# Optimization experiments

Hardware: AMD Instinct MI355X
Metric: run time of the kernel (lower is better)

The kernel has to match this reference:

```python
import jax, jax.numpy as jnp
import numpy as np
from jax import lax

B, L, DIM = 2, 2048, 2048
HK, HV = 16, 32
DK, DV = 128, 128
KCONV = 4
KEY_DIM = HK * DK          # 2048
VAL_DIM = HV * DV          # 4096
CONV_DIM = 2 * KEY_DIM + VAL_DIM  # 8192
EPS = 1e-6


def _l2norm(x, eps=1e-6):
    return x * lax.rsqrt((x * x).sum(-1, keepdims=True) + eps)


def _gated_delta_rule(q, k, v, g, beta):
    # q,k: (B,L,H,DK); v: (B,L,H,DV); g,beta: (B,L,H)
    q = _l2norm(q.astype(jnp.float32)) * (DK ** -0.5)
    k = _l2norm(k.astype(jnp.float32))
    v = v.astype(jnp.float32)
    g = g.astype(jnp.float32)
    beta = beta.astype(jnp.float32)
    # time-major for scan: (L,B,H,...)
    qs = q.transpose(1, 0, 2, 3)
    ks = k.transpose(1, 0, 2, 3)
    vs = v.transpose(1, 0, 2, 3)
    gs = g.transpose(1, 0, 2)
    bs = beta.transpose(1, 0, 2)
    state0 = jnp.zeros((B, HV, DK, DV), jnp.float32)

    def step(state, inp):
        q_t, k_t, v_t, g_t, b_t = inp
        state = state * jnp.exp(g_t)[..., None, None]          # decay
        kv_mem = jnp.einsum('bhk,bhkv->bhv', k_t, state)       # read
        delta = (v_t - kv_mem) * b_t[..., None]                # error-correct
        state = state + jnp.einsum('bhk,bhv->bhkv', k_t, delta)
        out_t = jnp.einsum('bhk,bhkv->bhv', q_t, state)
        return state, out_t

    _, outs = lax.scan(step, state0, (qs, ks, vs, gs, bs))
    return outs.transpose(1, 0, 2, 3)  # (B,L,H,DV)


def setup_inputs() -> dict:
    key = jax.random.key(0)
    ks = jax.random.split(key, 8)
    s = 0.02
    return {
        'x': jax.random.normal(ks[0], (B, L, DIM), jnp.float32),
        'W_qkv': jax.random.normal(ks[1], (CONV_DIM, DIM), jnp.float32) * s,
        'W_z': jax.random.normal(ks[2], (VAL_DIM, DIM), jnp.float32) * s,
        'W_a': jax.random.normal(ks[3], (HV, DIM), jnp.float32) * s,
        'W_b': jax.random.normal(ks[4], (HV, DIM), jnp.float32) * s,
        'conv_w': jax.random.normal(ks[5], (CONV_DIM, 1, KCONV), jnp.float32) * 0.2,
        'A_log': jnp.log(jax.random.uniform(ks[6], (HV,), jnp.float32, 1e-6, 16.0)),
        'dt_bias': jnp.ones((HV,), jnp.float32),
        'norm_weight': jnp.ones((DV,), jnp.float32),
        'W_out': jax.random.normal(ks[7], (DIM, VAL_DIM), jnp.float32) * s,
    }


def reference(x, W_qkv, W_z, W_a, W_b, conv_w, A_log, dt_bias, norm_weight, W_out):
    qkv = x @ W_qkv.T                      # (B,L,CONV_DIM)
    z = x @ W_z.T                          # (B,L,VAL_DIM)
    a = x @ W_a.T                          # (B,L,HV)
    b = x @ W_b.T                          # (B,L,HV)
    # depthwise causal conv1d (left pad K-1)
    h = qkv.transpose(0, 2, 1)             # (B,C,L)
    h = lax.conv_general_dilated(h, conv_w, window_strides=(1,),
                                 padding=[(KCONV - 1, 0)],
                                 dimension_numbers=('NCH', 'OIH', 'NCH'),
                                 feature_group_count=CONV_DIM)
    qkv = jax.nn.silu(h.transpose(0, 2, 1))
    q, k, v = jnp.split(qkv, [KEY_DIM, 2 * KEY_DIM], axis=-1)
    q = q.reshape(B, L, HK, DK)
    k = k.reshape(B, L, HK, DK)
    v = v.reshape(B, L, HV, DV)
    rep = HV // HK
    if rep > 1:
        q = jnp.repeat(q, rep, axis=2)
        k = jnp.repeat(k, rep, axis=2)
    g = -jnp.exp(A_log.astype(jnp.float32)) * jax.nn.softplus(a.astype(jnp.float32) + dt_bias)
    beta = jax.nn.sigmoid(b)
    out = _gated_delta_rule(q, k, v, g, beta)   # (B,L,HV,DV) fp32
    # gated RMSNorm over DV: silu(z) * weight * norm(out)
    var = (out * out).mean(-1, keepdims=True)
    out = out * lax.rsqrt(var + EPS) * norm_weight
    zg = z.reshape(B, L, HV, DV)
    out = out * jax.nn.silu(zg.astype(jnp.float32))
    out = out.astype(x.dtype).reshape(B, L, VAL_DIM)
    return out @ W_out.T
```

## Files before the change

### kernel.cpp

```cpp
#include <hip/hip_runtime.h>
#include <hip/hip_bf16.h>
#include <cstddef>
#include <cstdint>

constexpr int B = 2, L = 2048, DIM = 2048;
constexpr int HK = 16, HV = 32, DK = 128, DV = 128;
constexpr int KEY_DIM = HK * DK;
constexpr int VAL_DIM = HV * DV;
constexpr int CONV_DIM = 2 * KEY_DIM + VAL_DIM;
constexpr int NPROJ = CONV_DIM + VAL_DIM + HV + HV;
constexpr int NPAD  = ((NPROJ + 255) / 256) * 256;
constexpr size_t ROWS = (size_t)B * L;
constexpr float EPS = 1e-6f;
constexpr int CHUNK = 64, NCHUNK = L / CHUNK;
constexpr int NCH_TOT = B * HV * NCHUNK;
constexpr int CONV_LT = 8;
constexpr int CONV_TL = L / CONV_LT;

constexpr size_t OFF_QKV  = 0;
constexpr size_t OFF_Z    = OFF_QKV + ROWS * CONV_DIM * 2;
constexpr size_t OFF_A    = OFF_Z   + ROWS * VAL_DIM * 2;
constexpr size_t OFF_B    = OFF_A   + ROWS * HV * 4;
constexpr size_t OFF_G    = OFF_B   + ROWS * HV * 4;
constexpr size_t OFF_BETA = OFF_G   + ROWS * HV * 4;
constexpr size_t OFF_U    = OFF_BETA + ROWS * HV * 4;
constexpr size_t OFF_WQK  = OFF_U + (size_t)NCH_TOT * CHUNK * DV * 4;
constexpr size_t OFF_HALO = OFF_WQK + (size_t)NCH_TOT * CHUNK * CHUNK * 2;
constexpr size_t WS_NEED_BYTES = OFF_HALO + (size_t)3 * B * CONV_LT * CONV_DIM * 2;
constexpr size_t OFF_WCAT = OFF_U;
constexpr size_t OFF_XB   = OFF_WQK;
constexpr size_t OFF_WOB  = OFF_U;
static_assert((size_t)NPAD * DIM * 2 <= (size_t)NCH_TOT * CHUNK * DV * 4, "Wcat fits U");

__device__ __forceinline__ float bf2f(unsigned short u) {
    union { float f; uint32_t i; } c; c.i = ((uint32_t)u) << 16; return c.f;
}
__device__ __forceinline__ unsigned short f2bf(float f) {
    union { float f; uint32_t u; } c; c.f = f;
    uint32_t u = c.u + 0x7FFFu + ((c.u >> 16) & 1u);
    return (unsigned short)(u >> 16);
}
__device__ __forceinline__ uint32_t pk2(float a, float b) {
    return (uint32_t)f2bf(a) | ((uint32_t)f2bf(b) << 16);
}

typedef __attribute__((ext_vector_type(8))) short bfrag;
typedef __attribute__((ext_vector_type(4))) float ffrag;

__device__ __forceinline__ void gload16(const unsigned short* g, unsigned short* l) {
    __builtin_amdgcn_global_load_lds(
        (const __attribute__((address_space(1))) uint32_t*)g,
        (__attribute__((address_space(3))) uint32_t*)l, 16, 0, 0);
}

__device__ __forceinline__ const float* w_row_multi(int n, const float* Wq, const float* Wz,
                                                    const float* Wa, const float* Wb) {
    if (n < CONV_DIM)                return Wq + (size_t)n * DIM;
    if (n < CONV_DIM + VAL_DIM)      return Wz + (size_t)(n - CONV_DIM) * DIM;
    if (n < CONV_DIM + VAL_DIM + HV) return Wa + (size_t)(n - CONV_DIM - VAL_DIM) * DIM;
    return Wb + (size_t)(n - CONV_DIM - VAL_DIM - HV) * DIM;
}

__global__ __launch_bounds__(256) void cvt_wcat(
    const float* __restrict__ Wq, const float* __restrict__ Wz,
    const float* __restrict__ Wa, const float* __restrict__ Wb,
    unsigned short* __restrict__ dst)
{
    const int r = blockIdx.x;
    const int c = threadIdx.x * 8;
    uint4 o;
    if (r < NPROJ) {
        const float* s = w_row_multi(r, Wq, Wz, Wa, Wb) + c;
        float4 v0 = *(const float4*)s;
        float4 v1 = *(const float4*)(s + 4);
        o = make_uint4(pk2(v0.x, v0.y), pk2(v0.z, v0.w), pk2(v1.x, v1.y), pk2(v1.z, v1.w));
    } else {
        o = make_uint4(0u, 0u, 0u, 0u);
    }
    *(uint4*)&dst[(size_t)r * DIM + c] = o;
}

__global__ __launch_bounds__(256) void cvt_f32bf(const float* __restrict__ src,
                                                 unsigned short* __restrict__ dst, int cols)
{
    const size_t r = blockIdx.x;
    for (int c = threadIdx.x * 8; c < cols; c += 256 * 8) {
        const float* s = src + r * cols + c;
        float4 v0 = *(const float4*)s;
        float4 v1 = *(const float4*)(s + 4);
        *(uint4*)&dst[r * cols + c] =
            make_uint4(pk2(v0.x, v0.y), pk2(v0.z, v0.w), pk2(v1.x, v1.y), pk2(v1.z, v1.w));
    }
}

__device__ __forceinline__ void store_multi(int m, int n, float v,
                                            unsigned short* qkv, unsigned short* z,
                                            float* a, float* b) {
    if (n < CONV_DIM) {
        qkv[(size_t)m * CONV_DIM + n] = f2bf(v);
    } else if (n < CONV_DIM + VAL_DIM) {
        z[(size_t)m * VAL_DIM + (n - CONV_DIM)] = f2bf(v);
    } else if (n < CONV_DIM + VAL_DIM + HV) {
        a[(size_t)m * HV + (n - CONV_DIM - VAL_DIM)] = v;
    } else if (n < NPROJ) {
        b[(size_t)m * HV + (n - CONV_DIM - VAL_DIM - HV)] = v;
    }
}

constexpr int BK = 64;

__global__ __launch_bounds__(512, 2) void gemm_inproj_bf(
    const unsigned short* __restrict__ xb,
    const unsigned short* __restrict__ Wcat,
    unsigned short* __restrict__ qkv, unsigned short* __restrict__ z,
    float* __restrict__ a_out, float* __restrict__ b_out)
{
    extern __shared__ __align__(16) unsigned short lds[];

    constexpr int NBX = NPAD / 256;
    constexpr int NB  = NBX * 16;
    const int id  = blockIdx.x;
    const int swz = (id & 7) * (NB >> 3) + (id >> 3);
    const int bx  = swz >> 4;
    const int by  = swz & 15;
    const int row0 = by * 256;
    const int col0 = bx * 256;

    const int t = threadIdx.x, lane = t & 63, wid = t >> 6;
    const int wr = wid >> 2, wc = wid & 3;
    const int quad = lane >> 4, l16 = lane & 15;

    ffrag acc[8][4];
#pragma unroll
    for (int i = 0; i < 8; ++i)
#pragma unroll
        for (int j = 0; j < 4; ++j) acc[i][j] = (ffrag)0.f;

    const int srow  = t >> 3;
    const int sslot = t & 7;
    const int scol  = ((sslot ^ (srow & 7)) * 8);
    const unsigned short* aS = xb   + (size_t)(row0 + srow) * DIM + scol;
    const unsigned short* bS = Wcat + (size_t)(col0 + srow) * DIM + scol;
    unsigned short* aD0 = lds + (wid * 8) * 64;
    unsigned short* bD0 = lds + 32768 + (wid * 8) * 64;

    const int x7 = l16 & 7;

    auto STAGE = [&](int buf, int k0) {
        unsigned short* aD = aD0 + buf * 16384;
        unsigned short* bD = bD0 + buf * 16384;
#pragma unroll
        for (int j = 0; j < 4; ++j) {
            gload16(aS + (size_t)(j * 64) * DIM + k0, aD + j * 64 * 64);
            gload16(bS + (size_t)(j * 64) * DIM + k0, bD + j * 64 * 64);
        }
    };

    auto COMPUTE = [&](int buf) {
        const unsigned short* A  = lds + buf * 16384;
        const unsigned short* Bm = lds + 32768 + buf * 16384;
#pragma unroll
        for (int kk = 0; kk < 2; ++kk) {
            const int so = ((kk * 4 + quad) ^ x7) * 8;
            bfrag aF[8], bF[4];
#pragma unroll
            for (int m = 0; m < 8; ++m)
                aF[m] = *(const bfrag*)&A[(wr * 128 + m * 16 + l16) * 64 + so];
#pragma unroll
            for (int n = 0; n < 4; ++n)
                bF[n] = *(const bfrag*)&Bm[(wc * 64 + n * 16 + l16) * 64 + so];
#pragma unroll
            for (int m = 0; m < 8; ++m)
#pragma unroll
                for (int n = 0; n < 4; ++n)
                    acc[m][n] = __builtin_amdgcn_mfma_f32_16x16x32_bf16(
                        aF[m], bF[n], acc[m][n], 0, 0, 0);
        }
    };

    STAGE(0, 0);
    __syncthreads();
    for (int kt = 0; kt < DIM / BK; ++kt) {
        if (kt + 1 < DIM / BK) STAGE((kt + 1) & 1, (kt + 1) * BK);
        COMPUTE(kt & 1);
        __syncthreads();
    }

#pragma unroll
    for (int m = 0; m < 8; ++m)
#pragma unroll
        for (int n = 0; n < 4; ++n) {
            int gr = row0 + wr * 128 + m * 16 + quad * 4;
            int gc = col0 + wc * 64 + n * 16 + l16;
#pragma unroll
            for (int reg = 0; reg < 4; ++reg)
                store_multi(gr + reg, gc, acc[m][n][reg], qkv, z, a_out, b_out);
        }
}

__global__ __launch_bounds__(256) void gemm_outproj_bf(
    const unsigned short* __restrict__ A,
    const unsigned short* __restrict__ Wb,
    float* __restrict__ C)
{
    __shared__ __align__(16) unsigned short As[2][128 * BK];
    __shared__ __align__(16) unsigned short Bs[2][128 * BK];

    constexpr int NB = (ROWS / 128) * (DIM / 128);
    const int id  = blockIdx.x;
    const int swz = (id & 7) * (NB >> 3) + (id >> 3);
    const int bx  = swz >> 5;
    const int by  = swz & 31;
    const int row0 = by * 128;
    const int col0 = bx * 128;

    const int t = threadIdx.x, lane = t & 63, wid = t >> 6;
    const int quad = lane >> 4, l16 = lane & 15;
    const int wm = (wid >> 1) * 64, wn = (wid & 1) * 64;

    ffrag acc[4][4];
#pragma unroll
    for (int i = 0; i < 4; ++i)
#pragma unroll
        for (int j = 0; j < 4; ++j) acc[i][j] = (ffrag)0.f;

    const int srow  = t >> 3;
    const int sslot = t & 7;
    const int scol  = ((sslot ^ (srow & 7)) * 8);
    const unsigned short* aS = A  + (size_t)(row0 + srow) * VAL_DIM + scol;
    const unsigned short* bS = Wb + (size_t)(col0 + srow) * VAL_DIM + scol;

    const int aBase = (wm + l16) * BK;
    const int bBase = (wn + l16) * BK;
    const int x7 = l16 & 7;

    auto STAGE = [&](int buf, int k0) {
        unsigned short* aD = &As[buf][(wid * 8) * 64];
        unsigned short* bD = &Bs[buf][(wid * 8) * 64];
#pragma unroll
        for (int j = 0; j < 4; ++j) {
            gload16(aS + (size_t)(j * 32) * VAL_DIM + k0, aD + j * 32 * 64);
            gload16(bS + (size_t)(j * 32) * VAL_DIM + k0, bD + j * 32 * 64);
        }
    };

    auto COMPUTE = [&](int buf) {
#pragma unroll
        for (int kk = 0; kk < 2; ++kk) {
            const int so = ((kk * 4 + quad) ^ x7) * 8;
            bfrag aF[4], bF[4];
#pragma unroll
            for (int mt = 0; mt < 4; ++mt) aF[mt] = *(const bfrag*)&As[buf][aBase + mt * 16 * BK + so];
#pragma unroll
            for (int nt = 0; nt < 4; ++nt) bF[nt] = *(const bfrag*)&Bs[buf][bBase + nt * 16 * BK + so];
#pragma unroll
            for (int mt = 0; mt < 4; ++mt)
#pragma unroll
                for (int nt = 0; nt < 4; ++nt)
                    acc[mt][nt] = __builtin_amdgcn_mfma_f32_16x16x32_bf16(
                        aF[mt], bF[nt], acc[mt][nt], 0, 0, 0);
        }
    };

    STAGE(0, 0);
    __syncthreads();
    for (int kt = 0; kt < VAL_DIM / BK; ++kt) {
        if (kt + 1 < VAL_DIM / BK) STAGE((kt + 1) & 1, (kt + 1) * BK);
        COMPUTE(kt & 1);
        __syncthreads();
    }

#pragma unroll
    for (int mt = 0; mt < 4; ++mt)
#pragma unroll
        for (int nt = 0; nt < 4; ++nt) {
            int gr = row0 + wm + mt * 16 + quad * 4;
            int gc = col0 + wn + nt * 16 + l16;
#pragma unroll
            for (int reg = 0; reg < 4; ++reg)
                C[(size_t)(gr + reg) * DIM + gc] = acc[mt][nt][reg];
        }
}

__global__ __launch_bounds__(256) void conv_halo(const unsigned short* __restrict__ qkv,
                                                 unsigned short* __restrict__ hbuf)
{
    int idx = blockIdx.x * 256 + threadIdx.x;
    int c    = idx & (CONV_DIM - 1);
    int tile = (idx >> 13) & (CONV_LT - 1);
    int b    = idx >> 16;
    int l0 = tile * CONV_TL;
    const unsigned short* p = qkv + (size_t)b * L * CONV_DIM + c;
#pragma unroll
    for (int j = 0; j < 3; ++j) {
        unsigned short v = (tile > 0) ? p[(size_t)(l0 - 3 + j) * CONV_DIM] : (unsigned short)0;
        hbuf[((size_t)j * B * CONV_LT + b * CONV_LT + tile) * CONV_DIM + c] = v;
    }
}

__global__ __launch_bounds__(256) void conv_silu(unsigned short* __restrict__ qkv,
                                                 const float* __restrict__ conv_w,
                                                 const unsigned short* __restrict__ hbuf)
{
    int idx = blockIdx.x * 256 + threadIdx.x;
    int c    = idx & (CONV_DIM - 1);
    int tile = (idx >> 13) & (CONV_LT - 1);
    int b    = idx >> 16;
    const float w0 = conv_w[c * 4 + 0];
    const float w1 = conv_w[c * 4 + 1];
    const float w2 = conv_w[c * 4 + 2];
    const float w3 = conv_w[c * 4 + 3];
    unsigned short* p = qkv + ((size_t)b * L + tile * CONV_TL) * CONV_DIM + c;
    const size_t hb = (size_t)b * CONV_LT + tile;
    float x0 = bf2f(hbuf[((size_t)0 * B * CONV_LT + hb) * CONV_DIM + c]);
    float x1 = bf2f(hbuf[((size_t)1 * B * CONV_LT + hb) * CONV_DIM + c]);
    float x2 = bf2f(hbuf[((size_t)2 * B * CONV_LT + hb) * CONV_DIM + c]);
    for (int l0 = 0; l0 < CONV_TL; l0 += 8) {
        float xv[8];
#pragma unroll
        for (int j = 0; j < 8; ++j) xv[j] = bf2f(p[(size_t)(l0 + j) * CONV_DIM]);
#pragma unroll
        for (int j = 0; j < 8; ++j) {
            float h = w0 * x0 + w1 * x1 + w2 * x2 + w3 * xv[j];
            float s = h / (1.f + __expf(-h));
            p[(size_t)(l0 + j) * CONV_DIM] = f2bf(s);
            x0 = x1; x1 = x2; x2 = xv[j];
        }
    }
}

__global__ __launch_bounds__(256) void normqk(unsigned short* __restrict__ qkv)
{
    int wid  = blockIdx.x * 4 + (threadIdx.x >> 6);
    int lane = threadIdx.x & 63;
    int hk  = wid & 15;
    int sel = (wid >> 4) & 1;
    int row = wid >> 5;
    unsigned short* p = qkv + (size_t)row * CONV_DIM + sel * KEY_DIM + hk * DK;
    float x0 = bf2f(p[lane]), x1 = bf2f(p[lane + 64]);
    float ss = x0 * x0 + x1 * x1;
#pragma unroll
    for (int o = 32; o >= 1; o >>= 1) ss += __shfl_xor(ss, o);
    float sc = rsqrtf(ss + 1e-6f);
    if (sel == 0) sc *= 0.08838834764831845f;
    p[lane]      = f2bf(x0 * sc);
    p[lane + 64] = f2bf(x1 * sc);
}

__global__ __launch_bounds__(256) void gatecoef(const float* __restrict__ a_buf,
                                                const float* __restrict__ b_buf,
                                                const float* __restrict__ A_log,
                                                const float* __restrict__ dt_bias,
                                                float* __restrict__ glog,
                                                float* __restrict__ beta)
{
    int idx = blockIdx.x * blockDim.x + threadIdx.x;
    int h = idx & (HV - 1);
    float av = a_buf[idx];
    float bv = b_buf[idx];
    float x  = av + dt_bias[h];
    float sp = (x > 20.f) ? x : log1pf(__expf(x));
    glog[idx] = -__expf(A_log[h]) * sp;
    beta[idx] = 1.f / (1.f + __expf(-bv));
}


constexpr int RSK  = 136;
constexpr int RST  = 72;
constexpr int RSTD = 68;
constexpr int RSR1 = 260;

constexpr int P1_oKs  = 0;
constexpr int P1_oQs  = P1_oKs + 64 * RSK * 2;
constexpr int P1_oDT  = 0;
constexpr int P1_oAf  = P1_oQs + 64 * RSK * 2;
constexpr int P1_oRHS = P1_oAf + 64 * RST * 2;
constexpr int P1_oG   = P1_oRHS + 64 * RSR1 * 4;
constexpr int P1_oEG  = P1_oG + 256;
constexpr int P1_oBs  = P1_oEG + 256;
constexpr int P1_SMEM = P1_oBs + 256;

__global__ __launch_bounds__(256, 1) void chunk_prep(
    unsigned short* __restrict__ qkv,
    const float* __restrict__ glog,
    const float* __restrict__ beta,
    float* __restrict__ Ubuf,
    unsigned short* __restrict__ Wqkbuf)
{
    extern __shared__ __align__(16) char smem[];
    unsigned short* sKs = (unsigned short*)(smem + P1_oKs);
    unsigned short* sQs = (unsigned short*)(smem + P1_oQs);
    unsigned short* sDT = (unsigned short*)(smem + P1_oDT);
    unsigned short* sAf = (unsigned short*)(smem + P1_oAf);
    float* sRHS = (float*)(smem + P1_oRHS);
    float* sG   = (float*)(smem + P1_oG);
    float* sEG  = (float*)(smem + P1_oEG);
    float* sBs  = (float*)(smem + P1_oBs);

    const int bid = blockIdx.x;
    const int ch = bid & (NCHUNK - 1);
    const int h  = (bid >> 5) & (HV - 1);
    const int bb = bid >> 10;
    const int hk = h >> 1;
    const int t    = threadIdx.x;
    const int w    = t >> 6;
    const int lane = t & 63;
    const int quad = lane >> 4;
    const int l16  = lane & 15;
    const int quad8 = quad * 8;
    const size_t bL = (size_t)bb * L;
    const int l0 = ch * CHUNK;
    const int VOFF = 2 * KEY_DIM + h * DV;

    {
        const int r  = t >> 2;
        const int c0 = (t & 3) * 32;
        const unsigned short* grow = qkv + (bL + l0 + r) * CONV_DIM;
        const unsigned short* gq = grow + hk * DK + c0;
        const unsigned short* gk = grow + KEY_DIM + hk * DK + c0;
#pragma unroll
        for (int u = 0; u < 4; ++u) {
            *(uint4*)&sKs[r * RSK + c0 + 8 * u] = *(const uint4*)(gk + 8 * u);
            *(uint4*)&sQs[r * RSK + c0 + 8 * u] = *(const uint4*)(gq + 8 * u);
        }
        if (t < 64) {
            float gl = glog[(bL + l0 + t) * HV + h];
#pragma unroll
            for (int off = 1; off < 64; off <<= 1) {
                float v = __shfl_up(gl, off, 64);
                if (lane >= off) gl += v;
            }
            sG[t]  = gl;
            sEG[t] = __expf(gl);
            sBs[t] = beta[(bL + l0 + t) * HV + h];
        }
    }
    __syncthreads();

    {
        ffrag accA[4], accW[4];
#pragma unroll
        for (int mt = 0; mt < 4; ++mt) { accA[mt] = (ffrag)0.f; accW[mt] = (ffrag)0.f; }
#pragma unroll
        for (int kk = 0; kk < 4; ++kk) {
            bfrag bf = *(const bfrag*)&sKs[(16 * w + l16) * RSK + 32 * kk + quad8];
#pragma unroll
            for (int mt = 0; mt < 4; ++mt) {
                bfrag ak = *(const bfrag*)&sKs[(16 * mt + l16) * RSK + 32 * kk + quad8];
                bfrag aq = *(const bfrag*)&sQs[(16 * mt + l16) * RSK + 32 * kk + quad8];
                accA[mt] = __builtin_amdgcn_mfma_f32_16x16x32_bf16(ak, bf, accA[mt], 0, 0, 0);
                accW[mt] = __builtin_amdgcn_mfma_f32_16x16x32_bf16(aq, bf, accW[mt], 0, 0, 0);
            }
        }
        const int j = 16 * w + l16;
        const float gj = sG[j];
        unsigned short* Wqp = Wqkbuf + (size_t)bid * (CHUNK * CHUNK);
#pragma unroll
        for (int mt = 0; mt < 4; ++mt)
#pragma unroll
            for (int reg = 0; reg < 4; ++reg) {
                int i = 16 * mt + quad * 4 + reg;
                float sc = __expf(sG[i] - gj);
                sAf[i * RST + j] = f2bf((j < i) ? sBs[i] * sc * accA[mt][reg] : 0.f);
                Wqp[i * CHUNK + j] = f2bf((j <= i) ? sc * accW[mt][reg] : 0.f);
            }
    }

    {
        const int r  = t >> 2;
        const int c0 = (t & 3) * 32;
        const float be  = sBs[r];
        const float beg = be * sEG[r];
        const unsigned short* gv = qkv + (bL + l0 + r) * CONV_DIM + VOFF + c0;
#pragma unroll
        for (int u = 0; u < 4; ++u) {
            uint4 vv = *(const uint4*)(gv + 8 * u);
            const unsigned short* vp = (const unsigned short*)&vv;
#pragma unroll
            for (int e = 0; e < 8; ++e)
                sRHS[r * RSR1 + c0 + 8 * u + e] = be * bf2f(vp[e]);
        }
#pragma unroll
        for (int u = 0; u < 4; ++u)
#pragma unroll
            for (int e = 0; e < 8; ++e)
                sRHS[r * RSR1 + 128 + c0 + 8 * u + e] =
                    beg * bf2f(sKs[r * RSK + c0 + 8 * u + e]);
    }
    __syncthreads();

    for (int u = t; u < 256 * RSTD / 2; u += 256) ((uint32_t*)sDT)[u] = 0;

    float* Up = Ubuf + (size_t)bid * (CHUNK * DV);
    for (int sb = 0; sb < 4; ++sb) {
        const int sb16 = 16 * sb;
        if (sb > 0) {
            const int kbn = (sb + 1) >> 1;
            ffrag c16[4];
#pragma unroll
            for (int nt = 0; nt < 4; ++nt) c16[nt] = (ffrag)0.f;
            for (int kb = 0; kb < kbn; ++kb) {
                bfrag af = *(const bfrag*)&sAf[(sb16 + l16) * RST + 32 * kb + quad8];
#pragma unroll
                for (int nt = 0; nt < 4; ++nt) {
                    bfrag bf = *(const bfrag*)&sDT[(64 * w + 16 * nt + l16) * RSTD + 32 * kb + quad8];
                    c16[nt] = __builtin_amdgcn_mfma_f32_16x16x32_bf16(af, bf, c16[nt], 0, 0, 0);
                }
            }
#pragma unroll
            for (int nt = 0; nt < 4; ++nt)
#pragma unroll
                for (int reg = 0; reg < 4; ++reg)
                    sRHS[(sb16 + quad * 4 + reg) * RSR1 + 64 * w + 16 * nt + l16] -= c16[nt][reg];
        }
        __syncthreads();
        {
            const int c = t;
            float d16[16];
#pragma unroll
            for (int e = 0; e < 16; ++e) {
                const int i = sb16 + e;
                float acc = sRHS[i * RSR1 + c];
#pragma unroll
                for (int f = 0; f < 16; ++f)
                    if (f < e) acc -= bf2f(sAf[i * RST + sb16 + f]) * d16[f];
                d16[e] = acc;
            }
#pragma unroll
            for (int e = 0; e < 16; e += 2)
                *(uint32_t*)&sDT[c * RSTD + sb16 + e] = pk2(d16[e], d16[e + 1]);
            if (c < 128) {
                float* up = Up + c;
#pragma unroll
                for (int e = 0; e < 16; ++e) up[(size_t)(sb16 + e) * DV] = d16[e];
            } else {
                unsigned short* wp = qkv + (bL + l0 + sb16) * CONV_DIM + VOFF + (c - 128);
#pragma unroll
                for (int e = 0; e < 16; ++e) wp[(size_t)e * CONV_DIM] = f2bf(-d16[e]);
            }
        }
        __syncthreads();
    }
}

constexpr int P2_oSTb = 0;
constexpr int P2_oWk  = P2_oSTb + 128 * RSK * 2;
constexpr int P2_oQs  = P2_oWk + 64 * RSK * 2;
constexpr int P2_oKT  = P2_oQs + 64 * RSK * 2;
constexpr int P2_oWqk = P2_oKT + 128 * RST * 2;
constexpr int P2_oDT  = P2_oWqk + 64 * RST * 2;
constexpr int P2_oDdT = P2_oDT + 128 * RST * 2;
constexpr int P2_oEG  = P2_oDdT + 128 * RST * 2;
constexpr int P2_oEGd = P2_oEG + 256;
constexpr int P2_oNW  = P2_oEGd + 256;
constexpr int P2_oP   = P2_oNW + 512;
constexpr int P2_SMEM = P2_oP + 512;

__global__ __launch_bounds__(512, 1) void chunk_scan2(
    const unsigned short* __restrict__ qkv,
    const float* __restrict__ glog,
    const float* __restrict__ Ubuf,
    const unsigned short* __restrict__ Wqkbuf,
    unsigned short* __restrict__ z_io,
    const float* __restrict__ norm_w)
{
    extern __shared__ __align__(16) char smem[];
    unsigned short* sSTb = (unsigned short*)(smem + P2_oSTb);
    unsigned short* sWk  = (unsigned short*)(smem + P2_oWk);
    unsigned short* sQs  = (unsigned short*)(smem + P2_oQs);
    unsigned short* sKT  = (unsigned short*)(smem + P2_oKT);
    unsigned short* sWqk = (unsigned short*)(smem + P2_oWqk);
    unsigned short* sDT  = (unsigned short*)(smem + P2_oDT);
    unsigned short* sDdT = (unsigned short*)(smem + P2_oDdT);
    float* sEG  = (float*)(smem + P2_oEG);
    float* sEGd = (float*)(smem + P2_oEGd);
    float* sNW  = (float*)(smem + P2_oNW);
    float* sP   = (float*)(smem + P2_oP);

    const int bb = blockIdx.x >> 5;
    const int h  = blockIdx.x & (HV - 1);
    const int hk = h >> 1;
    const int t    = threadIdx.x;
    const int w    = t >> 6;
    const int lane = t & 63;
    const int quad = lane >> 4;
    const int l16  = lane & 15;
    const int quad8 = quad * 8;
    const int rg = w >> 1;
    const int dh = w & 1;
    const size_t bL = (size_t)bb * L;
    const int VOFF = 2 * KEY_DIM + h * DV;
    const size_t chbase0 = ((size_t)bb * HV + h) * NCHUNK;

    const int r  = t >> 3;
    const int c0 = (t & 7) * 16;
    const int cw = (t & 7) * 8;

    ffrag accS[8];
#pragma unroll
    for (int nt = 0; nt < 8; ++nt) accS[nt] = (ffrag)0.f;

    for (int u = t; u < 64 * RSK; u += 512) ((uint32_t*)sSTb)[u] = 0;
    if (t < 128) sNW[t] = norm_w[t];

    uint4 pQ[2], pK[2], pWk[2], pWqk;
    float pGl;

    auto PF = [&](int ch) {
        const int l0p = ch * CHUNK;
        const unsigned short* grow = qkv + (bL + l0p + r) * CONV_DIM;
        const unsigned short* gq = grow + hk * DK + c0;
        const unsigned short* gk = grow + KEY_DIM + hk * DK + c0;
        const unsigned short* gw = grow + VOFF + c0;
#pragma unroll
        for (int u = 0; u < 2; ++u) {
            pQ[u]  = *(const uint4*)(gq + 8 * u);
            pK[u]  = *(const uint4*)(gk + 8 * u);
            pWk[u] = *(const uint4*)(gw + 8 * u);
        }
        pWqk = *(const uint4*)(Wqkbuf + (chbase0 + ch) * (CHUNK * CHUNK) + r * CHUNK + cw);
        pGl = glog[(bL + l0p + (t & 63)) * HV + h];
    };

    PF(0);

    for (int ch = 0; ch < NCHUNK; ++ch) {
        const int l0 = ch * CHUNK;
        const size_t cb = chbase0 + ch;
        __syncthreads();

        ffrag accD[4];
        {
            const float* up = Ubuf + cb * (CHUNK * DV) + (size_t)(quad * 4) * DV + 16 * w + l16;
#pragma unroll
            for (int mt = 0; mt < 4; ++mt)
#pragma unroll
                for (int reg = 0; reg < 4; ++reg)
                    accD[mt][reg] = up[(size_t)(16 * mt + reg) * DV];
        }
        unsigned short pz[4][4];
        {
            const unsigned short* zp =
                z_io + (bL + l0 + 16 * rg + quad * 4) * (size_t)VAL_DIM + h * DV + 64 * dh + l16;
#pragma unroll
            for (int nt = 0; nt < 4; ++nt)
#pragma unroll
                for (int reg = 0; reg < 4; ++reg)
                    pz[nt][reg] = zp[(size_t)reg * VAL_DIM + 16 * nt];
        }

#pragma unroll
        for (int u = 0; u < 2; ++u) {
            *(uint4*)&sQs[r * RSK + c0 + 8 * u] = pQ[u];
            *(uint4*)&sWk[r * RSK + c0 + 8 * u] = pWk[u];
            const unsigned short* kp = (const unsigned short*)&pK[u];
#pragma unroll
            for (int e = 0; e < 8; ++e) {
                const int c = c0 + 8 * u + e;
                sKT[c * RST + ((((r >> 3) ^ (c >> 3)) & 7) << 3) + (r & 7)] = kp[e];
            }
        }
        *(uint4*)&sWqk[r * RST + cw] = pWqk;

        {
            float gl = pGl;
            if (t < 64) {
#pragma unroll
                for (int off = 1; off < 64; off <<= 1) {
                    float v = __shfl_up(gl, off, 64);
                    if (lane >= off) gl += v;
                }
                float gc = __shfl(gl, 63, 64);
                sEG[t]  = __expf(gl);
                sEGd[t] = __expf(gc - gl);
            }
        }

        if (ch + 1 < NCHUNK) PF(ch + 1);
        __syncthreads();

#pragma unroll
        for (int kk = 0; kk < 4; ++kk) {
            bfrag b0 = *(const bfrag*)&sSTb[(16 * w + l16) * RSK + 32 * kk + quad8];
#pragma unroll
            for (int mt = 0; mt < 4; ++mt) {
                bfrag af = *(const bfrag*)&sWk[(16 * mt + l16) * RSK + 32 * kk + quad8];
                accD[mt] = __builtin_amdgcn_mfma_f32_16x16x32_bf16(af, b0, accD[mt], 0, 0, 0);
            }
        }

        {
            const int dv = 16 * w + l16;
#pragma unroll
            for (int mt = 0; mt < 4; ++mt) {
                const int i0 = 16 * mt + quad * 4;
                const float e0 = sEGd[i0], e1 = sEGd[i0 + 1], e2 = sEGd[i0 + 2], e3 = sEGd[i0 + 3];
                const float d0 = accD[mt][0], d1 = accD[mt][1];
                const float d2 = accD[mt][2], d3 = accD[mt][3];
                *(uint32_t*)&sDT[dv * RST + i0]      = pk2(d0, d1);
                *(uint32_t*)&sDT[dv * RST + i0 + 2]  = pk2(d2, d3);
                *(uint32_t*)&sDdT[dv * RST + i0]     = pk2(d0 * e0, d1 * e1);
                *(uint32_t*)&sDdT[dv * RST + i0 + 2] = pk2(d2 * e2, d3 * e3);
            }
        }
        __syncthreads();

        ffrag accO[4];
#pragma unroll
        for (int nt = 0; nt < 4; ++nt) accO[nt] = (ffrag)0.f;
#pragma unroll
        for (int kk = 0; kk < 4; ++kk) {
            bfrag af = *(const bfrag*)&sQs[(16 * rg + l16) * RSK + 32 * kk + quad8];
#pragma unroll
            for (int nt = 0; nt < 4; ++nt) {
                bfrag bf = *(const bfrag*)&sSTb[(64 * dh + 16 * nt + l16) * RSK + 32 * kk + quad8];
                accO[nt] = __builtin_amdgcn_mfma_f32_16x16x32_bf16(af, bf, accO[nt], 0, 0, 0);
            }
        }
#pragma unroll
        for (int nt = 0; nt < 4; ++nt)
#pragma unroll
            for (int reg = 0; reg < 4; ++reg)
                accO[nt][reg] *= sEG[16 * rg + quad * 4 + reg];
#pragma unroll
        for (int kk = 0; kk < 2; ++kk) {
            bfrag af = *(const bfrag*)&sWqk[(16 * rg + l16) * RST + 32 * kk + quad8];
#pragma unroll
            for (int nt = 0; nt < 4; ++nt) {
                bfrag bf = *(const bfrag*)&sDT[(64 * dh + 16 * nt + l16) * RST + 32 * kk + quad8];
                accO[nt] = __builtin_amdgcn_mfma_f32_16x16x32_bf16(af, bf, accO[nt], 0, 0, 0);
            }
        }

        float p4[4];
#pragma unroll
        for (int reg = 0; reg < 4; ++reg) {
            float p = 0.f;
#pragma unroll
            for (int nt = 0; nt < 4; ++nt) p += accO[nt][reg] * accO[nt][reg];
#pragma unroll
            for (int m = 1; m < 16; m <<= 1) p += __shfl_xor(p, m, 64);
            p4[reg] = p;
        }
        if (l16 == 0) {
#pragma unroll
            for (int reg = 0; reg < 4; ++reg) sP[w * 16 + quad * 4 + reg] = p4[reg];
        }

        {
            const float eGc = sEG[63];
#pragma unroll
            for (int nt = 0; nt < 8; ++nt)
#pragma unroll
                for (int reg = 0; reg < 4; ++reg) accS[nt][reg] *= eGc;
#pragma unroll
            for (int kk = 0; kk < 2; ++kk) {
                bfrag a0 = *(const bfrag*)&sDdT[(16 * w + l16) * RST + 32 * kk + quad8];
#pragma unroll
                for (int nt = 0; nt < 8; ++nt) {
                    const int ck = 16 * nt + l16;
                    bfrag bk = *(const bfrag*)&sKT[ck * RST +
                                 ((((4 * kk + quad) ^ (ck >> 3)) & 7) << 3)];
                    accS[nt] = __builtin_amdgcn_mfma_f32_16x16x32_bf16(a0, bk, accS[nt], 0, 0, 0);
                }
            }
        }
        __syncthreads();

        {
            float inv[4];
#pragma unroll
            for (int reg = 0; reg < 4; ++reg) {
                float pp = p4[reg] + sP[(w ^ 1) * 16 + quad * 4 + reg];
                inv[reg] = rsqrtf(pp * (1.f / 128.f) + EPS);
            }
            unsigned short* zw =
                z_io + (bL + l0 + 16 * rg + quad * 4) * (size_t)VAL_DIM + h * DV + 64 * dh + l16;
#pragma unroll
            for (int nt = 0; nt < 4; ++nt) {
                const float nwv = sNW[64 * dh + 16 * nt + l16];
#pragma unroll
                for (int reg = 0; reg < 4; ++reg) {
                    float zv = bf2f(pz[nt][reg]);
                    float y = accO[nt][reg] * inv[reg] * nwv * (zv / (1.f + __expf(-zv)));
                    zw[(size_t)reg * VAL_DIM + 16 * nt] = f2bf(y);
                }
            }
        }

#pragma unroll
        for (int nt = 0; nt < 8; ++nt)
#pragma unroll
            for (int reg = 0; reg < 4; ++reg)
                sSTb[(16 * w + quad * 4 + reg) * RSK + 16 * nt + l16] = f2bf(accS[nt][reg]);
    }
}

extern "C" void kernel_launch(void* const* d_in, const int* in_sizes, int n_in,
                              void* d_out, int out_size, void* d_ws, size_t ws_size,
                              hipStream_t stream)
{
    const float* x        = (const float*)d_in[0];
    const float* W_qkv    = (const float*)d_in[1];
    const float* W_z      = (const float*)d_in[2];
    const float* W_a      = (const float*)d_in[3];
    const float* W_b      = (const float*)d_in[4];
    const float* conv_w   = (const float*)d_in[5];
    const float* A_log    = (const float*)d_in[6];
    const float* dt_bias  = (const float*)d_in[7];
    const float* norm_w   = (const float*)d_in[8];
    const float* W_out    = (const float*)d_in[9];
    float* out = (float*)d_out;
    char*  ws  = (char*)d_ws;

    if (ws_size < WS_NEED_BYTES) return;

    unsigned short* qkv = (unsigned short*)(ws + OFF_QKV);
    unsigned short* z   = (unsigned short*)(ws + OFF_Z);
    float* a    = (float*)(ws + OFF_A);
    float* bbuf = (float*)(ws + OFF_B);
    float* gl   = (float*)(ws + OFF_G);
    float* beta = (float*)(ws + OFF_BETA);
    float* Ubuf = (float*)(ws + OFF_U);
    unsigned short* Wqkbuf = (unsigned short*)(ws + OFF_WQK);
    unsigned short* hbuf   = (unsigned short*)(ws + OFF_HALO);
    unsigned short* Wcat   = (unsigned short*)(ws + OFF_WCAT);
    unsigned short* xb     = (unsigned short*)(ws + OFF_XB);
    unsigned short* Wob    = (unsigned short*)(ws + OFF_WOB);

    static bool attr_set = false;
    if (!attr_set) {
        (void)hipFuncSetAttribute((const void*)chunk_prep,
                                  hipFuncAttributeMaxDynamicSharedMemorySize, P1_SMEM);
        (void)hipFuncSetAttribute((const void*)chunk_scan2,
                                  hipFuncAttributeMaxDynamicSharedMemorySize, P2_SMEM);
        (void)hipFuncSetAttribute((const void*)gemm_inproj_bf,
                                  hipFuncAttributeMaxDynamicSharedMemorySize, 131072);
        attr_set = true;
    }

    cvt_wcat<<<NPAD, 256, 0, stream>>>(W_qkv, W_z, W_a, W_b, Wcat);
    cvt_f32bf<<<(int)ROWS, 256, 0, stream>>>(x, xb, DIM);
    gemm_inproj_bf<<<(NPAD / 256) * 16, 512, 131072, stream>>>(xb, Wcat, qkv, z, a, bbuf);
    conv_halo<<<(B * CONV_LT * CONV_DIM) / 256, 256, 0, stream>>>(qkv, hbuf);
    conv_silu<<<(B * CONV_LT * CONV_DIM) / 256, 256, 0, stream>>>(qkv, conv_w, hbuf);
    normqk<<<(B * L * 2 * HK) / 4, 256, 0, stream>>>(qkv);
    gatecoef<<<(B * L * HV) / 256, 256, 0, stream>>>(a, bbuf, A_log, dt_bias, gl, beta);
    chunk_prep<<<NCH_TOT, 256, P1_SMEM, stream>>>(qkv, gl, beta, Ubuf, Wqkbuf);
    chunk_scan2<<<B * HV, 512, P2_SMEM, stream>>>(qkv, gl, Ubuf, Wqkbuf, z, norm_w);
    cvt_f32bf<<<DIM, 256, 0, stream>>>(W_out, Wob, VAL_DIM);
    gemm_outproj_bf<<<(ROWS / 128) * (DIM / 128), 256, 0, stream>>>(z, Wob, out);
}
```

Baseline: 966.3 us.

## Triple-buffer both GEMMs with 256x128 tiles and explicit vmcnt waits

Both the input-projection and output-projection GEMMs now use a 256x128 block tile with 512 threads and three LDS stages. Raw s_waitcnt/s_barrier replace __syncthreads so that two future k-tiles stay in flight while the current one is computed. The input GEMM moves from 256x256 tiles (128 accumulators per thread) to smaller tiles, which doubles the block count and lowers register pressure. In exchange, each block reuses less data and occupancy is capped at one block per CU.

```diff
diff --git a/kernel.cpp b/kernel.cpp
--- a/kernel.cpp
+++ b/kernel.cpp
@@ -109,7 +109,10 @@
 
 constexpr int BK = 64;
 
-__global__ __launch_bounds__(512, 2) void gemm_inproj_bf(
+constexpr int GBUF = 24576;
+constexpr int GEMM_SMEM = 3 * GBUF * 2;
+
+__global__ __launch_bounds__(512, 1) void gemm_inproj_bf(
     const unsigned short* __restrict__ xb,
     const unsigned short* __restrict__ Wcat,
     unsigned short* __restrict__ qkv, unsigned short* __restrict__ z,
@@ -117,60 +120,64 @@
 {
     extern __shared__ __align__(16) unsigned short lds[];
 
-    constexpr int NBX = NPAD / 256;
-    constexpr int NB  = NBX * 16;
+    constexpr int NT  = DIM / BK;
+    constexpr int NBY = (int)ROWS / 256;
+    constexpr int NBX = NPAD / 128;
+    constexpr int NB  = NBY * NBX;
     const int id  = blockIdx.x;
     const int swz = (id & 7) * (NB >> 3) + (id >> 3);
+    const int by  = swz & 15;
     const int bx  = swz >> 4;
-    const int by  = swz & 15;
     const int row0 = by * 256;
-    const int col0 = bx * 256;
+    const int col0 = bx * 128;
 
     const int t = threadIdx.x, lane = t & 63, wid = t >> 6;
-    const int wr = wid >> 2, wc = wid & 3;
+    const int wr = wid >> 1, wc = wid & 1;
     const int quad = lane >> 4, l16 = lane & 15;
-
-    ffrag acc[8][4];
-#pragma unroll
-    for (int i = 0; i < 8; ++i)
+    const int x7 = l16 & 7;
+
+    ffrag acc[4][4];
+#pragma unroll
+    for (int i = 0; i < 4; ++i)
 #pragma unroll
         for (int j = 0; j < 4; ++j) acc[i][j] = (ffrag)0.f;
 
-    const int srow  = t >> 3;
-    const int sslot = t & 7;
-    const int scol  = ((sslot ^ (srow & 7)) * 8);
+    const int srow = t >> 3;
+    const int scol = (((t & 7) ^ (srow & 7)) * 8);
     const unsigned short* aS = xb   + (size_t)(row0 + srow) * DIM + scol;
     const unsigned short* bS = Wcat + (size_t)(col0 + srow) * DIM + scol;
     unsigned short* aD0 = lds + (wid * 8) * 64;
-    unsigned short* bD0 = lds + 32768 + (wid * 8) * 64;
-
-    const int x7 = l16 & 7;
-
-    auto STAGE = [&](int buf, int k0) {
-        unsigned short* aD = aD0 + buf * 16384;
-        unsigned short* bD = bD0 + buf * 16384;
-#pragma unroll
-        for (int j = 0; j < 4; ++j) {
-            gload16(aS + (size_t)(j * 64) * DIM + k0, aD + j * 64 * 64);
-            gload16(bS + (size_t)(j * 64) * DIM + k0, bD + j * 64 * 64);
-        }
+    unsigned short* bD0 = lds + 16384 + (wid * 8) * 64;
+
+    auto STAGE = [&](int kt) {
+        const int b = kt % 3;
+        unsigned short* aD = aD0 + b * GBUF;
+        unsigned short* bD = bD0 + b * GBUF;
+        const int k0 = kt * BK;
+#pragma unroll
+        for (int g = 0; g < 4; ++g)
+            gload16(aS + (size_t)(g * 64) * DIM + k0, aD + g * 64 * 64);
+#pragma unroll
+        for (int g = 0; g < 2; ++g)
+            gload16(bS + (size_t)(g * 64) * DIM + k0, bD + g * 64 * 64);
     };
 
-    auto COMPUTE = [&](int buf) {
-        const unsigned short* A  = lds + buf * 16384;
-        const unsigned short* Bm = lds + 32768 + buf * 16384;
+    auto COMPUTE = [&](int kt) {
+        const int b = kt % 3;
+        const unsigned short* A  = lds + b * GBUF;
+        const unsigned short* Bm = lds + b * GBUF + 16384;
 #pragma unroll
         for (int kk = 0; kk < 2; ++kk) {
             const int so = ((kk * 4 + quad) ^ x7) * 8;
-            bfrag aF[8], bF[4];
-#pragma unroll
-            for (int m = 0; m < 8; ++m)
-                aF[m] = *(const bfrag*)&A[(wr * 128 + m * 16 + l16) * 64 + so];
+            bfrag aF[4], bF[4];
+#pragma unroll
+            for (int m = 0; m < 4; ++m)
+                aF[m] = *(const bfrag*)&A[(wr * 64 + m * 16 + l16) * 64 + so];
 #pragma unroll
             for (int n = 0; n < 4; ++n)
                 bF[n] = *(const bfrag*)&Bm[(wc * 64 + n * 16 + l16) * 64 + so];
 #pragma unroll
-            for (int m = 0; m < 8; ++m)
+            for (int m = 0; m < 4; ++m)
 #pragma unroll
                 for (int n = 0; n < 4; ++n)
                     acc[m][n] = __builtin_amdgcn_mfma_f32_16x16x32_bf16(
@@ -178,19 +185,28 @@
         }
     };
 
-    STAGE(0, 0);
-    __syncthreads();
-    for (int kt = 0; kt < DIM / BK; ++kt) {
-        if (kt + 1 < DIM / BK) STAGE((kt + 1) & 1, (kt + 1) * BK);
-        COMPUTE(kt & 1);
-        __syncthreads();
-    }
-
-#pragma unroll
-    for (int m = 0; m < 8; ++m)
+    STAGE(0); STAGE(1);
+    asm volatile("s_waitcnt vmcnt(6)" ::: "memory");
+    asm volatile("s_barrier" ::: "memory");
+    for (int kt = 0; kt < NT; ++kt) {
+        if (kt + 2 < NT) {
+            STAGE(kt + 2);
+            asm volatile("s_waitcnt vmcnt(12)" ::: "memory");
+        } else if (kt + 1 < NT) {
+            asm volatile("s_waitcnt vmcnt(6)" ::: "memory");
+        } else {
+            asm volatile("s_waitcnt vmcnt(0)" ::: "memory");
+        }
+        asm volatile("s_barrier" ::: "memory");
+        COMPUTE(kt);
+        asm volatile("s_barrier" ::: "memory");
+    }
+
+#pragma unroll
+    for (int m = 0; m < 4; ++m)
 #pragma unroll
         for (int n = 0; n < 4; ++n) {
-            int gr = row0 + wr * 128 + m * 16 + quad * 4;
+            int gr = row0 + wr * 64 + m * 16 + quad * 4;
             int gc = col0 + wc * 64 + n * 16 + l16;
 #pragma unroll
             for (int reg = 0; reg < 4; ++reg)
@@ -198,25 +214,28 @@
         }
 }
 
-__global__ __launch_bounds__(256) void gemm_outproj_bf(
+__global__ __launch_bounds__(512, 1) void gemm_outproj_bf(
     const unsigned short* __restrict__ A,
     const unsigned short* __restrict__ Wb,
     float* __restrict__ C)
 {
-    __shared__ __align__(16) unsigned short As[2][128 * BK];
-    __shared__ __align__(16) unsigned short Bs[2][128 * BK];
-
-    constexpr int NB = (ROWS / 128) * (DIM / 128);
+    extern __shared__ __align__(16) unsigned short lds[];
+
+    constexpr int NT  = VAL_DIM / BK;
+    constexpr int NBY = (int)ROWS / 256;
+    constexpr int NBX = DIM / 128;
+    constexpr int NB  = NBY * NBX;
     const int id  = blockIdx.x;
     const int swz = (id & 7) * (NB >> 3) + (id >> 3);
-    const int bx  = swz >> 5;
-    const int by  = swz & 31;
-    const int row0 = by * 128;
+    const int by  = swz & 15;
+    const int bx  = swz >> 4;
+    const int row0 = by * 256;
     const int col0 = bx * 128;
 
     const int t = threadIdx.x, lane = t & 63, wid = t >> 6;
+    const int wr = wid >> 1, wc = wid & 1;
     const int quad = lane >> 4, l16 = lane & 15;
-    const int wm = (wid >> 1) * 64, wn = (wid & 1) * 64;
+    const int x7 = l16 & 7;
 
     ffrag acc[4][4];
 #pragma unroll
@@ -224,61 +243,75 @@
 #pragma unroll
         for (int j = 0; j < 4; ++j) acc[i][j] = (ffrag)0.f;
 
-    const int srow  = t >> 3;
-    const int sslot = t & 7;
-    const int scol  = ((sslot ^ (srow & 7)) * 8);
+    const int srow = t >> 3;
+    const int scol = (((t & 7) ^ (srow & 7)) * 8);
     const unsigned short* aS = A  + (size_t)(row0 + srow) * VAL_DIM + scol;
     const unsigned short* bS = Wb + (size_t)(col0 + srow) * VAL_DIM + scol;
-
-    const int aBase = (wm + l16) * BK;
-    const int bBase = (wn + l16) * BK;
-    const int x7 = l16 & 7;
-
-    auto STAGE = [&](int buf, int k0) {
-        unsigned short* aD = &As[buf][(wid * 8) * 64];
-        unsigned short* bD = &Bs[buf][(wid * 8) * 64];
-#pragma unroll
-        for (int j = 0; j < 4; ++j) {
-            gload16(aS + (size_t)(j * 32) * VAL_DIM + k0, aD + j * 32 * 64);
-            gload16(bS + (size_t)(j * 32) * VAL_DIM + k0, bD + j * 32 * 64);
-        }
+    unsigned short* aD0 = lds + (wid * 8) * 64;
+    unsigned short* bD0 = lds + 16384 + (wid * 8) * 64;
+
+    auto STAGE = [&](int kt) {
+        const int b = kt % 3;
+        unsigned short* aD = aD0 + b * GBUF;
+        unsigned short* bD = bD0 + b * GBUF;
+        const int k0 = kt * BK;
+#pragma unroll
+        for (int g = 0; g < 4; ++g)
+            gload16(aS + (size_t)(g * 64) * VAL_DIM + k0, aD + g * 64 * 64);
+#pragma unroll
+        for (int g = 0; g < 2; ++g)
+            gload16(bS + (size_t)(g * 64) * VAL_DIM + k0, bD + g * 64 * 64);
     };
 
-    auto COMPUTE = [&](int buf) {
+    auto COMPUTE = [&](int kt) {
+        const int b = kt % 3;
+        const unsigned short* Am = lds + b * GBUF;
+        const unsigned short* Bm = lds + b * GBUF + 16384;
 #pragma unroll
         for (int kk = 0; kk < 2; ++kk) {
             const int so = ((kk * 4 + quad) ^ x7) * 8;
             bfrag aF[4], bF[4];
 #pragma unroll
-            for (int mt = 0; mt < 4; ++mt) aF[mt] = *(const bfrag*)&As[buf][aBase + mt * 16 * BK + so];
-#pragma unroll
-            for (int nt = 0; nt < 4; ++nt) bF[nt] = *(const bfrag*)&Bs[buf][bBase + nt * 16 * BK + so];
-#pragma unroll
-            for (int mt = 0; mt < 4; ++mt)
-#pragma unroll
-                for (int nt = 0; nt < 4; ++nt)
-                    acc[mt][nt] = __builtin_amdgcn_mfma_f32_16x16x32_bf16(
-                        aF[mt], bF[nt], acc[mt][nt], 0, 0, 0);
+            for (int m = 0; m < 4; ++m)
+                aF[m] = *(const bfrag*)&Am[(wr * 64 + m * 16 + l16) * 64 + so];
+#pragma unroll
+            for (int n = 0; n < 4; ++n)
+                bF[n] = *(const bfrag*)&Bm[(wc * 64 + n * 16 + l16) * 64 + so];
+#pragma unroll
+            for (int m = 0; m < 4; ++m)
+#pragma unroll
+                for (int n = 0; n < 4; ++n)
+                    acc[m][n] = __builtin_amdgcn_mfma_f32_16x16x32_bf16(
+                        aF[m], bF[n], acc[m][n], 0, 0, 0);
         }
     };
 
-    STAGE(0, 0);
-    __syncthreads();
-    for (int kt = 0; kt < VAL_DIM / BK; ++kt) {
-        if (kt + 1 < VAL_DIM / BK) STAGE((kt + 1) & 1, (kt + 1) * BK);
-        COMPUTE(kt & 1);
-        __syncthreads();
-    }
-
-#pragma unroll
-    for (int mt = 0; mt < 4; ++mt)
-#pragma unroll
-        for (int nt = 0; nt < 4; ++nt) {
-            int gr = row0 + wm + mt * 16 + quad * 4;
-            int gc = col0 + wn + nt * 16 + l16;
+    STAGE(0); STAGE(1);
+    asm volatile("s_waitcnt vmcnt(6)" ::: "memory");
+    asm volatile("s_barrier" ::: "memory");
+    for (int kt = 0; kt < NT; ++kt) {
+        if (kt + 2 < NT) {
+            STAGE(kt + 2);
+            asm volatile("s_waitcnt vmcnt(12)" ::: "memory");
+        } else if (kt + 1 < NT) {
+            asm volatile("s_waitcnt vmcnt(6)" ::: "memory");
+        } else {
+            asm volatile("s_waitcnt vmcnt(0)" ::: "memory");
+        }
+        asm volatile("s_barrier" ::: "memory");
+        COMPUTE(kt);
+        asm volatile("s_barrier" ::: "memory");
+    }
+
+#pragma unroll
+    for (int m = 0; m < 4; ++m)
+#pragma unroll
+        for (int n = 0; n < 4; ++n) {
+            int gr = row0 + wr * 64 + m * 16 + quad * 4;
+            int gc = col0 + wc * 64 + n * 16 + l16;
 #pragma unroll
             for (int reg = 0; reg < 4; ++reg)
-                C[(size_t)(gr + reg) * DIM + gc] = acc[mt][nt][reg];
+                C[(size_t)(gr + reg) * DIM + gc] = acc[m][n][reg];
         }
 }
 
@@ -835,13 +868,16 @@
         (void)hipFuncSetAttribute((const void*)chunk_scan2,
                                   hipFuncAttributeMaxDynamicSharedMemorySize, P2_SMEM);
         (void)hipFuncSetAttribute((const void*)gemm_inproj_bf,
-                                  hipFuncAttributeMaxDynamicSharedMemorySize, 131072);
+                                  hipFuncAttributeMaxDynamicSharedMemorySize, GEMM_SMEM);
+        (void)hipFuncSetAttribute((const void*)gemm_outproj_bf,
+                                  hipFuncAttributeMaxDynamicSharedMemorySize, GEMM_SMEM);
         attr_set = true;
     }
 
     cvt_wcat<<<NPAD, 256, 0, stream>>>(W_qkv, W_z, W_a, W_b, Wcat);
     cvt_f32bf<<<(int)ROWS, 256, 0, stream>>>(x, xb, DIM);
-    gemm_inproj_bf<<<(NPAD / 256) * 16, 512, 131072, stream>>>(xb, Wcat, qkv, z, a, bbuf);
+    gemm_inproj_bf<<<((int)ROWS / 256) * (NPAD / 128), 512, GEMM_SMEM, stream>>>(
+        xb, Wcat, qkv, z, a, bbuf);
     conv_halo<<<(B * CONV_LT * CONV_DIM) / 256, 256, 0, stream>>>(qkv, hbuf);
     conv_silu<<<(B * CONV_LT * CONV_DIM) / 256, 256, 0, stream>>>(qkv, conv_w, hbuf);
     normqk<<<(B * L * 2 * HK) / 4, 256, 0, stream>>>(qkv);
@@ -849,5 +885,5 @@
     chunk_prep<<<NCH_TOT, 256, P1_SMEM, stream>>>(qkv, gl, beta, Ubuf, Wqkbuf);
     chunk_scan2<<<B * HV, 512, P2_SMEM, stream>>>(qkv, gl, Ubuf, Wqkbuf, z, norm_w);
     cvt_f32bf<<<DIM, 256, 0, stream>>>(W_out, Wob, VAL_DIM);
-    gemm_outproj_bf<<<(ROWS / 128) * (DIM / 128), 256, 0, stream>>>(z, Wob, out);
-}
+    gemm_outproj_bf<<<((int)ROWS / 256) * (DIM / 128), 512, GEMM_SMEM, stream>>>(z, Wob, out);
+}
```

New measurement: 924.8 us. 1.04x faster.
